# Optimization experiments

Hardware: AMD Instinct MI355X
Metric: run time of the kernel (lower is better)

Reference implementation:

```python
import jax, jax.numpy as jnp
import numpy as np

B, N, DIN, DOUT = 8, 2048, 512, 512
EDGE_P = 0.01  # edge probability for the random binary adjacency


def setup_inputs() -> dict:
    key = jax.random.key(0)
    k1, k2, k3, k4 = jax.random.split(key, 4)
    inputs = jax.random.normal(k1, (B, N, DIN), dtype=jnp.float32)
    # binary dense adjacency (dense_to_sparse discards weights -> edges are adj != 0)
    adj = (jax.random.uniform(k2, (B, N, N)) < EDGE_P).astype(jnp.float32)
    W = jax.random.normal(k3, (DIN, DOUT), dtype=jnp.float32) / np.sqrt(DIN)
    b = jax.random.normal(k4, (DOUT,), dtype=jnp.float32) * 0.01
    return {"inputs": inputs, "adj": adj, "W": W, "b": b}


def _gcn_norm(adj):
    # binary edge mask (edge weights from dense_to_sparse are discarded)
    A = (adj != 0).astype(adj.dtype)
    # add remaining self-loops: force diagonal to 1
    eye = jnp.eye(A.shape[-1], dtype=A.dtype)
    A = jnp.maximum(A, eye)
    deg = A.sum(axis=-1)                       # [B, N]
    dinv = jnp.where(deg > 0, jax.lax.rsqrt(deg), 0.0)
    # D^-1/2 (A + I) D^-1/2
    return dinv[..., :, None] * A * dinv[..., None, :]


def reference(inputs, adj, W, b):
    norm = _gcn_norm(adj)                      # [B, N, N]
    h = jnp.einsum('bnf,fo->bno', inputs, W)   # linear (no internal bias)
    agg = jnp.einsum('bnm,bmo->bno', norm, h)  # degree-normalized aggregation
    return jnp.tanh(agg + b)
```

## Files before the change

### kernel.cpp

```cpp
#include <hip/hip_runtime.h>
#include <hip/hip_bf16.h>
#include <math.h>


#define NROWS 16384
#define NCOLS 2048
#define DF    512
#define CAP   64

typedef __attribute__((ext_vector_type(8))) short bf16x8;
typedef __attribute__((ext_vector_type(4))) float f32x4;
typedef const void __attribute__((address_space(1))) gvoid_t;
typedef void __attribute__((address_space(3))) svoid_t;

__global__ __launch_bounds__(256) void wt_kernel(
    const float* __restrict__ W, __hip_bfloat16* __restrict__ WT) {
  __shared__ float t[64][65];
  const int b2 = blockIdx.x;
  const int bx = b2 & 7, by = b2 >> 3;
  const int tid = threadIdx.x;
  const int tx = tid & 63, ty = tid >> 6;
  #pragma unroll
  for (int i = 0; i < 16; ++i)
    t[ty + i * 4][tx] = W[(size_t)(by * 64 + ty + i * 4) * DF + bx * 64 + tx];
  __syncthreads();
  #pragma unroll
  for (int i = 0; i < 16; ++i)
    WT[(size_t)(bx * 64 + ty + i * 4) * DF + by * 64 + tx] =
        __float2bfloat16(t[tx][ty + i * 4]);
}

__global__ __launch_bounds__(256) void fused_sg(
    const float* __restrict__ X, const __hip_bfloat16* __restrict__ WT,
    const float* __restrict__ adj, __hip_bfloat16* __restrict__ H,
    int* __restrict__ cnt, int* __restrict__ edges, float* __restrict__ dinv) {
  __shared__ __hip_bfloat16 As[2][128 * 32];
  __shared__ __hip_bfloat16 Bs[2][128 * 32];
  const int id = blockIdx.x;
  const int tid = threadIdx.x;
  const int lane = tid & 63;
  const int wv = tid >> 6;

  if (id < 512) {
    const int xcd = id & 7;
    const int jj = id >> 3;
    const int bm = (xcd * 16 + (jj >> 2)) * 128;
    const int bn = (jj & 3) * 128;
    const int w = wv;
    const int wm = (w >> 1) * 64;
    const int wn = (w & 1) * 64;
    const int srow = tid >> 2;
    const int scol = (tid & 3) * 8;
    const int arow = tid >> 1;
    const int akh  = (tid & 1) * 16;
    const int kl = (lane >> 4) * 8;
    const int rl = lane & 15;

    f32x4 acc[4][4] = {};
    float4 ar0, ar1, ar2, ar3;

    #define LOAD_A(k0)  do {                                                  \
      const float4* g_ = (const float4*)(X + (size_t)(bm + arow) * DF + (k0) + akh); \
      ar0 = g_[0]; ar1 = g_[1]; ar2 = g_[2]; ar3 = g_[3]; } while (0)

    #define STAGE_B(k0, buf)  do {                                            \
      _Pragma("unroll")                                                       \
      for (int i = 0; i < 2; ++i) {                                           \
        const __hip_bfloat16* gb = WT + (size_t)(bn + i * 64 + srow) * DF + (k0) + scol; \
        char* lb = (char*)&Bs[buf][0] + i * 4096 + w * 1024;                  \
        __builtin_amdgcn_global_load_lds((gvoid_t*)gb, (svoid_t*)lb, 16, 0, 0); \
      } } while (0)

    #define WRITE_A(buf)  do {                                               \
      float xs[16];                                                          \
      *(float4*)&xs[0] = ar0; *(float4*)&xs[4] = ar1;                        \
      *(float4*)&xs[8] = ar2; *(float4*)&xs[12] = ar3;                       \
      union { __hip_bfloat16 hh[16]; uint4 q[2]; } pk;                       \
      _Pragma("unroll")                                                      \
      for (int i = 0; i < 16; ++i) pk.hh[i] = __float2bfloat16(xs[i]);       \
      char* la = (char*)&As[buf][0] + arow * 64 + akh * 2;                   \
      ((uint4*)la)[0] = pk.q[0];                                             \
      ((uint4*)la)[1] = pk.q[1]; } while (0)

    LOAD_A(0);
    STAGE_B(0, 0);
    WRITE_A(0);
    __syncthreads();

    for (int t = 0; t < 16; ++t) {
      const int c_ = t & 1, nx = c_ ^ 1;
      if (t < 15) {
        LOAD_A((t + 1) * 32);
        STAGE_B((t + 1) * 32, nx);
      }
      bf16x8 af[4], bf[4];
      #pragma unroll
      for (int mi = 0; mi < 4; ++mi)
        af[mi] = *(const bf16x8*)&As[c_][(wm + mi * 16 + rl) * 32 + kl];
      #pragma unroll
      for (int ni = 0; ni < 4; ++ni)
        bf[ni] = *(const bf16x8*)&Bs[c_][(wn + ni * 16 + rl) * 32 + kl];
      #pragma unroll
      for (int mi = 0; mi < 4; ++mi)
        #pragma unroll
        for (int ni = 0; ni < 4; ++ni)
          acc[mi][ni] = __builtin_amdgcn_mfma_f32_16x16x32_bf16(af[mi], bf[ni], acc[mi][ni], 0, 0, 0);
      if (t < 15) WRITE_A(nx);
      __syncthreads();
    }

    const int rq = (lane >> 4) * 4;
    #pragma unroll
    for (int mi = 0; mi < 4; ++mi)
      #pragma unroll
      for (int ni = 0; ni < 4; ++ni) {
        const int col = bn + wn + ni * 16 + rl;
        #pragma unroll
        for (int j = 0; j < 4; ++j) {
          const int row = bm + wm + mi * 16 + rq + j;
          H[(size_t)row * DF + col] = __float2bfloat16(acc[mi][ni][j]);
        }
      }
    #undef LOAD_A
    #undef STAGE_B
    #undef WRITE_A
  } else {
    const int rbase = (id - 512) * 16 + wv * 4;
    float4 cur[8], nxt[8];
    {
      const float4* r4 = (const float4*)(adj + (size_t)rbase * NCOLS);
      #pragma unroll
      for (int k = 0; k < 8; ++k) cur[k] = r4[k * 64 + lane];
    }
    #pragma unroll
    for (int g = 0; g < 4; ++g) {
      const int r = rbase + g;
      if (g < 3) {
        const float4* rn = (const float4*)(adj + (size_t)(r + 1) * NCOLS);
        #pragma unroll
        for (int k = 0; k < 8; ++k) nxt[k] = rn[k * 64 + lane];
      }
      const int n = r & (NCOLS - 1);
      unsigned m = 0;
      #pragma unroll
      for (int k = 0; k < 8; ++k) {
        m |= (cur[k].x != 0.0f ? 1u : 0u) << (4 * k);
        m |= (cur[k].y != 0.0f ? 1u : 0u) << (4 * k + 1);
        m |= (cur[k].z != 0.0f ? 1u : 0u) << (4 * k + 2);
        m |= (cur[k].w != 0.0f ? 1u : 0u) << (4 * k + 3);
      }
      if (lane == ((n >> 2) & 63))
        m |= 1u << (((n >> 8) << 2) | (n & 3));
      const int c_ = __popc(m);
      int inc = c_;
      #pragma unroll
      for (int off = 1; off < 64; off <<= 1) {
        const int tv = __shfl_up(inc, off);
        if (lane >= off) inc += tv;
      }
      const int tot = __shfl(inc, 63);
      int p = inc - c_;
      unsigned mm = m;
      const size_t eb = (size_t)r * CAP;
      while (mm) {
        const int bpos = __ffs(mm) - 1;
        mm &= mm - 1;
        if (p < CAP)
          edges[eb + p] = ((bpos >> 2) << 8) + (lane << 2) + (bpos & 3);
        ++p;
      }
      if (lane == 63) {
        cnt[r] = tot < CAP ? tot : CAP;
        dinv[r] = rsqrtf((float)tot);
      }
      #pragma unroll
      for (int k = 0; k < 8; ++k) cur[k] = nxt[k];
    }
  }
}

__device__ __forceinline__ float fast_tanh(float x) {
  const float t = __expf(2.0f * x);
  return 1.0f - __fdividef(2.0f, t + 1.0f);
}

__global__ __launch_bounds__(256) void aggregate(
    const __hip_bfloat16* __restrict__ h, const int* __restrict__ cnt,
    const int* __restrict__ edges, const float* __restrict__ dinv,
    const float* __restrict__ bias, float* __restrict__ out) {
  const int lane = threadIdx.x & 63;
  const int wv = threadIdx.x >> 6;
  const int batch = blockIdx.x & 7;
  const int qb = blockIdx.x >> 3;
  const int rn = qb * 4 + wv;
  const int r = (batch << 11) + rn;
  const int c = cnt[r];
  const float* dv = dinv + (batch << 11);
  const uint4* hbase = (const uint4*)(h + (size_t)(batch << 11) * DF);
  const int* eb = edges + (size_t)r * CAP;

  float acc[8] = {0.f,0.f,0.f,0.f,0.f,0.f,0.f,0.f};
  for (int e = 0; e < c; e += 8) {
    int   mj[8];
    float wj[8];
    uint4 vj[8];
    #pragma unroll
    for (int j = 0; j < 8; ++j)
      if (e + j < c) mj[j] = eb[e + j];
    #pragma unroll
    for (int j = 0; j < 8; ++j)
      if (e + j < c) {
        wj[j] = dv[mj[j]];
        vj[j] = hbase[(size_t)mj[j] * 64 + lane];
      }
    #pragma unroll
    for (int j = 0; j < 8; ++j)
      if (e + j < c) {
        const float wt = wj[j];
        acc[0] += wt * __uint_as_float(vj[j].x << 16);
        acc[1] += wt * __uint_as_float(vj[j].x & 0xffff0000u);
        acc[2] += wt * __uint_as_float(vj[j].y << 16);
        acc[3] += wt * __uint_as_float(vj[j].y & 0xffff0000u);
        acc[4] += wt * __uint_as_float(vj[j].z << 16);
        acc[5] += wt * __uint_as_float(vj[j].z & 0xffff0000u);
        acc[6] += wt * __uint_as_float(vj[j].w << 16);
        acc[7] += wt * __uint_as_float(vj[j].w & 0xffff0000u);
      }
  }
  const float4* b4 = (const float4*)bias;
  const float4 bb0 = b4[lane * 2];
  const float4 bb1 = b4[lane * 2 + 1];
  const float dn = dv[rn];
  float4 o;
  float* op = out + (size_t)r * DF + lane * 8;
  o.x = fast_tanh(acc[0] * dn + bb0.x);
  o.y = fast_tanh(acc[1] * dn + bb0.y);
  o.z = fast_tanh(acc[2] * dn + bb0.z);
  o.w = fast_tanh(acc[3] * dn + bb0.w);
  *(float4*)op = o;
  o.x = fast_tanh(acc[4] * dn + bb1.x);
  o.y = fast_tanh(acc[5] * dn + bb1.y);
  o.z = fast_tanh(acc[6] * dn + bb1.z);
  o.w = fast_tanh(acc[7] * dn + bb1.w);
  *(float4*)(op + 4) = o;
}

extern "C" void kernel_launch(void* const* d_in, const int* in_sizes, int n_in,
                              void* d_out, int out_size, void* d_ws, size_t ws_size,
                              hipStream_t stream) {
  const float* X    = (const float*)d_in[0];
  const float* adj  = (const float*)d_in[1];
  const float* W    = (const float*)d_in[2];
  const float* bias = (const float*)d_in[3];
  float* out = (float*)d_out;

  char* ws = (char*)d_ws;
  __hip_bfloat16* h    = (__hip_bfloat16*)(ws);
  __hip_bfloat16* WT   = (__hip_bfloat16*)(ws + 16777216);
  float*          dinv = (float*)(ws + 17301504);
  int*            cnt  = (int*)  (ws + 17367040);
  int*            edges= (int*)  (ws + 17432576);

  wt_kernel<<<64, 256, 0, stream>>>(W, WT);
  fused_sg<<<1536, 256, 0, stream>>>(X, WT, adj, h, cnt, edges, dinv);
  aggregate<<<4096, 256, 0, stream>>>(h, cnt, edges, dinv, bias, out);
}
```

Measured before the change: 76.53 us.

## Move adjacency scan into the W-transpose kernel and shrink GEMM tiles

The adjacency scan moves out of the fused GEMM kernel and into the weight-transpose launch, so the scan now runs alongside the transpose instead of competing with the GEMM blocks. The GEMM becomes its own kernel with 64x128 tiles and 1024 blocks in place of 128x128 tiles and 512 blocks. This is meant to improve load balance and occupancy. The cost is that the adjacency scan no longer overlaps with GEMM compute, and smaller tiles mean less data reuse.

New measurement: 70.34 us, median of 2. 8.1% less time.

```diff
diff --git a/kernel.cpp b/kernel.cpp
--- a/kernel.cpp
+++ b/kernel.cpp
@@ -13,170 +13,168 @@
 typedef const void __attribute__((address_space(1))) gvoid_t;
 typedef void __attribute__((address_space(3))) svoid_t;
 
-__global__ __launch_bounds__(256) void wt_kernel(
-    const float* __restrict__ W, __hip_bfloat16* __restrict__ WT) {
+__global__ __launch_bounds__(256) void scan_wt(
+    const float* __restrict__ W, __hip_bfloat16* __restrict__ WT,
+    const float* __restrict__ adj, int* __restrict__ cnt,
+    int* __restrict__ edges, float* __restrict__ dinv) {
   __shared__ float t[64][65];
-  const int b2 = blockIdx.x;
-  const int bx = b2 & 7, by = b2 >> 3;
+  const int blk = blockIdx.x;
   const int tid = threadIdx.x;
-  const int tx = tid & 63, ty = tid >> 6;
+  if (blk < 64) {
+    const int bx = blk & 7, by = blk >> 3;
+    const int tx = tid & 63, ty = tid >> 6;
+    #pragma unroll
+    for (int i = 0; i < 16; ++i)
+      t[ty + i * 4][tx] = W[(size_t)(by * 64 + ty + i * 4) * DF + bx * 64 + tx];
+    __syncthreads();
+    #pragma unroll
+    for (int i = 0; i < 16; ++i)
+      WT[(size_t)(bx * 64 + ty + i * 4) * DF + by * 64 + tx] =
+          __float2bfloat16(t[tx][ty + i * 4]);
+    return;
+  }
+  const int lane = tid & 63;
+  const int wv = tid >> 6;
+  const int rbase = (blk - 64) * 16 + wv * 4;
+  float4 cur[8], nxt[8];
+  {
+    const float4* r4 = (const float4*)(adj + (size_t)rbase * NCOLS);
+    #pragma unroll
+    for (int k = 0; k < 8; ++k) cur[k] = r4[k * 64 + lane];
+  }
   #pragma unroll
-  for (int i = 0; i < 16; ++i)
-    t[ty + i * 4][tx] = W[(size_t)(by * 64 + ty + i * 4) * DF + bx * 64 + tx];
-  __syncthreads();
-  #pragma unroll
-  for (int i = 0; i < 16; ++i)
-    WT[(size_t)(bx * 64 + ty + i * 4) * DF + by * 64 + tx] =
-        __float2bfloat16(t[tx][ty + i * 4]);
-}
-
-__global__ __launch_bounds__(256) void fused_sg(
+  for (int g = 0; g < 4; ++g) {
+    const int r = rbase + g;
+    if (g < 3) {
+      const float4* rn = (const float4*)(adj + (size_t)(r + 1) * NCOLS);
+      #pragma unroll
+      for (int k = 0; k < 8; ++k) nxt[k] = rn[k * 64 + lane];
+    }
+    const int n = r & (NCOLS - 1);
+    unsigned m = 0;
+    #pragma unroll
+    for (int k = 0; k < 8; ++k) {
+      m |= (cur[k].x != 0.0f ? 1u : 0u) << (4 * k);
+      m |= (cur[k].y != 0.0f ? 1u : 0u) << (4 * k + 1);
+      m |= (cur[k].z != 0.0f ? 1u : 0u) << (4 * k + 2);
+      m |= (cur[k].w != 0.0f ? 1u : 0u) << (4 * k + 3);
+    }
+    if (lane == ((n >> 2) & 63))
+      m |= 1u << (((n >> 8) << 2) | (n & 3));
+    const int c_ = __popc(m);
+    int inc = c_;
+    #pragma unroll
+    for (int off = 1; off < 64; off <<= 1) {
+      const int tv = __shfl_up(inc, off);
+      if (lane >= off) inc += tv;
+    }
+    const int tot = __shfl(inc, 63);
+    int p = inc - c_;
+    unsigned mm = m;
+    const size_t eb = (size_t)r * CAP;
+    while (mm) {
+      const int bpos = __ffs(mm) - 1;
+      mm &= mm - 1;
+      if (p < CAP)
+        edges[eb + p] = ((bpos >> 2) << 8) + (lane << 2) + (bpos & 3);
+      ++p;
+    }
+    if (lane == 63) {
+      cnt[r] = tot < CAP ? tot : CAP;
+      dinv[r] = rsqrtf((float)tot);
+    }
+    #pragma unroll
+    for (int k = 0; k < 8; ++k) cur[k] = nxt[k];
+  }
+}
+
+__global__ __launch_bounds__(256) void gemm_k(
     const float* __restrict__ X, const __hip_bfloat16* __restrict__ WT,
-    const float* __restrict__ adj, __hip_bfloat16* __restrict__ H,
-    int* __restrict__ cnt, int* __restrict__ edges, float* __restrict__ dinv) {
-  __shared__ __hip_bfloat16 As[2][128 * 32];
+    __hip_bfloat16* __restrict__ H) {
+  __shared__ __hip_bfloat16 As[2][64 * 32];
   __shared__ __hip_bfloat16 Bs[2][128 * 32];
-  const int id = blockIdx.x;
   const int tid = threadIdx.x;
   const int lane = tid & 63;
-  const int wv = tid >> 6;
-
-  if (id < 512) {
-    const int xcd = id & 7;
-    const int jj = id >> 3;
-    const int bm = (xcd * 16 + (jj >> 2)) * 128;
-    const int bn = (jj & 3) * 128;
-    const int w = wv;
-    const int wm = (w >> 1) * 64;
-    const int wn = (w & 1) * 64;
-    const int srow = tid >> 2;
-    const int scol = (tid & 3) * 8;
-    const int arow = tid >> 1;
-    const int akh  = (tid & 1) * 16;
-    const int kl = (lane >> 4) * 8;
-    const int rl = lane & 15;
-
-    f32x4 acc[4][4] = {};
-    float4 ar0, ar1, ar2, ar3;
-
-    #define LOAD_A(k0)  do {                                                  \
-      const float4* g_ = (const float4*)(X + (size_t)(bm + arow) * DF + (k0) + akh); \
-      ar0 = g_[0]; ar1 = g_[1]; ar2 = g_[2]; ar3 = g_[3]; } while (0)
-
-    #define STAGE_B(k0, buf)  do {                                            \
-      _Pragma("unroll")                                                       \
-      for (int i = 0; i < 2; ++i) {                                           \
-        const __hip_bfloat16* gb = WT + (size_t)(bn + i * 64 + srow) * DF + (k0) + scol; \
-        char* lb = (char*)&Bs[buf][0] + i * 4096 + w * 1024;                  \
-        __builtin_amdgcn_global_load_lds((gvoid_t*)gb, (svoid_t*)lb, 16, 0, 0); \
-      } } while (0)
-
-    #define WRITE_A(buf)  do {                                               \
-      float xs[16];                                                          \
-      *(float4*)&xs[0] = ar0; *(float4*)&xs[4] = ar1;                        \
-      *(float4*)&xs[8] = ar2; *(float4*)&xs[12] = ar3;                       \
-      union { __hip_bfloat16 hh[16]; uint4 q[2]; } pk;                       \
-      _Pragma("unroll")                                                      \
-      for (int i = 0; i < 16; ++i) pk.hh[i] = __float2bfloat16(xs[i]);       \
-      char* la = (char*)&As[buf][0] + arow * 64 + akh * 2;                   \
-      ((uint4*)la)[0] = pk.q[0];                                             \
-      ((uint4*)la)[1] = pk.q[1]; } while (0)
-
-    LOAD_A(0);
-    STAGE_B(0, 0);
-    WRITE_A(0);
-    __syncthreads();
-
-    for (int t = 0; t < 16; ++t) {
-      const int c_ = t & 1, nx = c_ ^ 1;
-      if (t < 15) {
-        LOAD_A((t + 1) * 32);
-        STAGE_B((t + 1) * 32, nx);
-      }
-      bf16x8 af[4], bf[4];
-      #pragma unroll
-      for (int mi = 0; mi < 4; ++mi)
-        af[mi] = *(const bf16x8*)&As[c_][(wm + mi * 16 + rl) * 32 + kl];
+  const int w = tid >> 6;
+  const int id = blockIdx.x;
+  const int xcd = id & 7;
+  const int q = id >> 3;
+  const int bm = (xcd * 32 + (q >> 2)) * 64;
+  const int bn = (q & 3) * 128;
+
+  const int wm = (w >> 1) * 32;
+  const int wn = (w & 1) * 64;
+  const int srow = tid >> 2;
+  const int scol = (tid & 3) * 8;
+  const int kl = (lane >> 4) * 8;
+  const int rl = lane & 15;
+
+  f32x4 acc[2][4] = {};
+  float4 ar0, ar1;
+
+  #define LOAD_A(k0)  do {                                              \
+    const float4* g_ = (const float4*)(X + (size_t)(bm + srow) * DF + (k0) + scol); \
+    ar0 = g_[0]; ar1 = g_[1]; } while (0)
+
+  #define STAGE_B(k0, buf)  do {                                        \
+    _Pragma("unroll")                                                   \
+    for (int i = 0; i < 2; ++i) {                                       \
+      const __hip_bfloat16* gb = WT + (size_t)(bn + i * 64 + srow) * DF + (k0) + scol; \
+      char* lb = (char*)&Bs[buf][0] + i * 4096 + w * 1024;              \
+      __builtin_amdgcn_global_load_lds((gvoid_t*)gb, (svoid_t*)lb, 16, 0, 0); \
+    } } while (0)
+
+  #define WRITE_A(buf)  do {                                            \
+    float xs[8];                                                        \
+    *(float4*)&xs[0] = ar0; *(float4*)&xs[4] = ar1;                     \
+    union { __hip_bfloat16 hh[8]; uint4 q_; } pk;                       \
+    _Pragma("unroll")                                                   \
+    for (int i = 0; i < 8; ++i) pk.hh[i] = __float2bfloat16(xs[i]);     \
+    char* la = (char*)&As[buf][0] + srow * 64 + scol * 2;               \
+    *(uint4*)la = pk.q_; } while (0)
+
+  LOAD_A(0);
+  STAGE_B(0, 0);
+  WRITE_A(0);
+  __syncthreads();
+
+  for (int t = 0; t < 16; ++t) {
+    const int c_ = t & 1, nx = c_ ^ 1;
+    if (t < 15) {
+      LOAD_A((t + 1) * 32);
+      STAGE_B((t + 1) * 32, nx);
+    }
+    bf16x8 af[2], bf[4];
+    #pragma unroll
+    for (int mi = 0; mi < 2; ++mi)
+      af[mi] = *(const bf16x8*)&As[c_][(wm + mi * 16 + rl) * 32 + kl];
+    #pragma unroll
+    for (int ni = 0; ni < 4; ++ni)
+      bf[ni] = *(const bf16x8*)&Bs[c_][(wn + ni * 16 + rl) * 32 + kl];
+    #pragma unroll
+    for (int mi = 0; mi < 2; ++mi)
       #pragma unroll
       for (int ni = 0; ni < 4; ++ni)
-        bf[ni] = *(const bf16x8*)&Bs[c_][(wn + ni * 16 + rl) * 32 + kl];
+        acc[mi][ni] = __builtin_amdgcn_mfma_f32_16x16x32_bf16(af[mi], bf[ni], acc[mi][ni], 0, 0, 0);
+    if (t < 15) WRITE_A(nx);
+    __syncthreads();
+  }
+
+  const int rq = (lane >> 4) * 4;
+  #pragma unroll
+  for (int mi = 0; mi < 2; ++mi)
+    #pragma unroll
+    for (int ni = 0; ni < 4; ++ni) {
+      const int col = bn + wn + ni * 16 + rl;
       #pragma unroll
-      for (int mi = 0; mi < 4; ++mi)
-        #pragma unroll
-        for (int ni = 0; ni < 4; ++ni)
-          acc[mi][ni] = __builtin_amdgcn_mfma_f32_16x16x32_bf16(af[mi], bf[ni], acc[mi][ni], 0, 0, 0);
-      if (t < 15) WRITE_A(nx);
-      __syncthreads();
-    }
-
-    const int rq = (lane >> 4) * 4;
-    #pragma unroll
-    for (int mi = 0; mi < 4; ++mi)
-      #pragma unroll
-      for (int ni = 0; ni < 4; ++ni) {
-        const int col = bn + wn + ni * 16 + rl;
-        #pragma unroll
-        for (int j = 0; j < 4; ++j) {
-          const int row = bm + wm + mi * 16 + rq + j;
-          H[(size_t)row * DF + col] = __float2bfloat16(acc[mi][ni][j]);
-        }
+      for (int j = 0; j < 4; ++j) {
+        const int row = bm + wm + mi * 16 + rq + j;
+        H[(size_t)row * DF + col] = __float2bfloat16(acc[mi][ni][j]);
       }
-    #undef LOAD_A
-    #undef STAGE_B
-    #undef WRITE_A
-  } else {
-    const int rbase = (id - 512) * 16 + wv * 4;
-    float4 cur[8], nxt[8];
-    {
-      const float4* r4 = (const float4*)(adj + (size_t)rbase * NCOLS);
-      #pragma unroll
-      for (int k = 0; k < 8; ++k) cur[k] = r4[k * 64 + lane];
-    }
-    #pragma unroll
-    for (int g = 0; g < 4; ++g) {
-      const int r = rbase + g;
-      if (g < 3) {
-        const float4* rn = (const float4*)(adj + (size_t)(r + 1) * NCOLS);
-        #pragma unroll
-        for (int k = 0; k < 8; ++k) nxt[k] = rn[k * 64 + lane];
-      }
-      const int n = r & (NCOLS - 1);
-      unsigned m = 0;
-      #pragma unroll
-      for (int k = 0; k < 8; ++k) {
-        m |= (cur[k].x != 0.0f ? 1u : 0u) << (4 * k);
-        m |= (cur[k].y != 0.0f ? 1u : 0u) << (4 * k + 1);
-        m |= (cur[k].z != 0.0f ? 1u : 0u) << (4 * k + 2);
-        m |= (cur[k].w != 0.0f ? 1u : 0u) << (4 * k + 3);
-      }
-      if (lane == ((n >> 2) & 63))
-        m |= 1u << (((n >> 8) << 2) | (n & 3));
-      const int c_ = __popc(m);
-      int inc = c_;
-      #pragma unroll
-      for (int off = 1; off < 64; off <<= 1) {
-        const int tv = __shfl_up(inc, off);
-        if (lane >= off) inc += tv;
-      }
-      const int tot = __shfl(inc, 63);
-      int p = inc - c_;
-      unsigned mm = m;
-      const size_t eb = (size_t)r * CAP;
-      while (mm) {
-        const int bpos = __ffs(mm) - 1;
-        mm &= mm - 1;
-        if (p < CAP)
-          edges[eb + p] = ((bpos >> 2) << 8) + (lane << 2) + (bpos & 3);
-        ++p;
-      }
-      if (lane == 63) {
-        cnt[r] = tot < CAP ? tot : CAP;
-        dinv[r] = rsqrtf((float)tot);
-      }
-      #pragma unroll
-      for (int k = 0; k < 8; ++k) cur[k] = nxt[k];
-    }
-  }
+    }
+  #undef LOAD_A
+  #undef STAGE_B
+  #undef WRITE_A
 }
 
 __device__ __forceinline__ float fast_tanh(float x) {
@@ -261,7 +259,7 @@
   int*            cnt  = (int*)  (ws + 17367040);
   int*            edges= (int*)  (ws + 17432576);
 
-  wt_kernel<<<64, 256, 0, stream>>>(W, WT);
-  fused_sg<<<1536, 256, 0, stream>>>(X, WT, adj, h, cnt, edges, dinv);
+  scan_wt<<<1088, 256, 0, stream>>>(W, WT, adj, cnt, edges, dinv);
+  gemm_k<<<1024, 256, 0, stream>>>(X, WT, h);
   aggregate<<<4096, 256, 0, stream>>>(h, cnt, edges, dinv, bias, out);
 }
```
